# Kernel tuning notes

Measured on AMD Instinct MI355X. Metric: run time of the kernel, lower is better.

Reference implementation:

```python
import jax, jax.numpy as jnp
import numpy as np

B, T, C, H, D, W = 4, 4096, 1024, 16, 64, 128  # batch, seq, n_embd, n_head, head_dim, window
NB = T // W  # number of query blocks
EPS = 1e-6


def _rms(x, w):
    # RMSNorm over last dim
    return x * jax.lax.rsqrt(jnp.mean(x * x, axis=-1, keepdims=True) + EPS) * w


def _rope(x, pos_ids):
    # MRoPE: pos_ids [T,3]; axis_id maps each freq to one of 3 axes
    inv_freq = 1.0 / (1e6 ** (jnp.arange(0, D, 2, dtype=jnp.float32) / D))  # [D/2]
    axis_id = jnp.arange(D // 2) % 3
    positions = pos_ids[:, axis_id].astype(jnp.float32)  # [T, D/2]
    freqs = positions * inv_freq  # [T, D/2]
    emb = jnp.concatenate([freqs, freqs], axis=-1)  # [T, D]
    cos = jnp.cos(emb)[None, None]  # [1,1,T,D]
    sin = jnp.sin(emb)[None, None]
    x1, x2 = x[..., : D // 2], x[..., D // 2 :]
    rot = jnp.concatenate([-x2, x1], axis=-1)
    return x * cos + rot * sin


def setup_inputs() -> dict:
    key = jax.random.key(0)
    ks = jax.random.split(key, 3)
    x = jax.random.normal(ks[0], (B, T, C), jnp.float32)
    pos = jnp.arange(T, dtype=jnp.int32)
    pos_ids = jnp.stack([pos, pos, pos], axis=-1)  # [T,3] text positions
    w_attn = jax.random.normal(ks[1], (C, C + 2 * D), jnp.float32) * 0.02
    w_proj = jax.random.normal(ks[2], (C, C), jnp.float32) * 0.02
    q_norm_w = jnp.ones((D,), jnp.float32)
    k_norm_w = jnp.ones((D,), jnp.float32)
    return {"x": x, "pos_ids": pos_ids, "w_attn": w_attn, "w_proj": w_proj,
            "q_norm_w": q_norm_w, "k_norm_w": k_norm_w}


def reference(x, pos_ids, w_attn, w_proj, q_norm_w, k_norm_w):
    # fused qkv projection (torch Linear without bias; weight stored [in,out])
    qkv = x @ w_attn  # [B,T,C+2D]
    q = qkv[..., :C].reshape(B, T, H, D).transpose(0, 2, 1, 3)  # [B,H,T,D]
    k = qkv[..., C : C + D][:, None]  # [B,1,T,D] single KV head (MQA)
    v = qkv[..., C + D :][:, None]  # [B,1,T,D]
    q = _rope(_rms(q, q_norm_w), pos_ids)
    k = _rope(_rms(k, k_norm_w), pos_ids)
    # sliding-window attention (q >= kv and q - kv <= W), computed in blocks of W
    qb = q.reshape(B, H, NB, W, D)
    kb = k.reshape(B, NB, W, D)
    vb = v.reshape(B, NB, W, D)
    kp = jnp.concatenate([jnp.zeros_like(kb[:, :1]), kb[:, :-1]], axis=1)  # prev k block
    vp = jnp.concatenate([jnp.zeros_like(vb[:, :1]), vb[:, :-1]], axis=1)
    kv_k = jnp.concatenate([kp, kb], axis=2)  # [B,NB,2W,D]
    kv_v = jnp.concatenate([vp, vb], axis=2)
    n = jnp.arange(NB)[:, None, None]
    qr = jnp.arange(W)[None, :, None]
    kr = jnp.arange(2 * W)[None, None, :]
    q_abs = n * W + qr
    kv_abs = (n - 1) * W + kr
    mask = (q_abs >= kv_abs) & (q_abs - kv_abs <= W) & (kv_abs >= 0)  # [NB,W,2W]
    scores = jnp.einsum("bhnqd,bnkd->bhnqk", qb, kv_k) / jnp.sqrt(jnp.float32(D))
    scores = jnp.where(mask[None, None], scores, -1e30)
    attn = jax.nn.softmax(scores, axis=-1)
    y = jnp.einsum("bhnqk,bnkd->bhnqd", attn, kv_v)  # [B,H,NB,W,D]
    y = y.reshape(B, H, T, D).transpose(0, 2, 1, 3).reshape(B, T, C)
    return y @ w_proj
```

## Files before the change

### kernel.cpp

```cpp
#include <hip/hip_runtime.h>


typedef __attribute__((ext_vector_type(8))) short short8;
typedef __attribute__((ext_vector_type(4))) float f32x4;
typedef __attribute__((ext_vector_type(16))) float f32x16;
typedef __attribute__((ext_vector_type(4))) unsigned uint4v;

#define DEV static __device__ __forceinline__

DEV unsigned short f2bf(float f) {
  unsigned u = __builtin_bit_cast(unsigned, f);
  u += 0x7fffu + ((u >> 16) & 1u);
  return (unsigned short)(u >> 16);
}
DEV float bf2f(unsigned short s) {
  unsigned u = ((unsigned)s) << 16;
  return __builtin_bit_cast(float, u);
}
DEV unsigned cvtpk(float a, float b) {
  unsigned r;
  asm("v_cvt_pk_bf16_f32 %0, %1, %2" : "=v"(r) : "v"(a), "v"(b));
  return r;
}

DEV f32x4 mfma16(short8 a, short8 b, f32x4 c) {
  return __builtin_amdgcn_mfma_f32_16x16x32_bf16(a, b, c, 0, 0, 0);
}
DEV f32x16 mfma32(short8 a, short8 b, f32x16 c) {
  return __builtin_amdgcn_mfma_f32_32x32x16_bf16(a, b, c, 0, 0, 0);
}

DEV void gload16(const void* g, void* l) {
  __builtin_amdgcn_global_load_lds(
      (const __attribute__((address_space(1))) unsigned int*)(unsigned long long)g,
      (__attribute__((address_space(3))) unsigned int*)(unsigned int)(unsigned long long)l,
      16, 0, 0);
}

#define BARRIER __builtin_amdgcn_s_barrier()
#define LGKM0  asm volatile("s_waitcnt lgkmcnt(0)" ::: "memory")
#define VMCNT4 asm volatile("s_waitcnt vmcnt(4)" ::: "memory")

__global__ __launch_bounds__(256) void k_cvt(const float* __restrict__ in,
                                             short* __restrict__ out, int n4) {
  int i = blockIdx.x * 256 + threadIdx.x;
  if (i >= n4) return;
  float4 v = ((const float4*)in)[i];
  short4 o;
  o.x = (short)f2bf(v.x); o.y = (short)f2bf(v.y);
  o.z = (short)f2bf(v.z); o.w = (short)f2bf(v.w);
  ((short4*)out)[i] = o;
}

__global__ __launch_bounds__(256) void k_tcvt(const float* __restrict__ W,
                                              short* __restrict__ Wt, int K, int N) {
  __shared__ float tl[32][33];
  int tx = threadIdx.x & 31, ty = threadIdx.x >> 5;
  int k0 = blockIdx.x * 32, n0 = blockIdx.y * 32;
#pragma unroll
  for (int i = 0; i < 4; ++i)
    tl[ty + i * 8][tx] = W[(size_t)(k0 + ty + i * 8) * N + n0 + tx];
  __syncthreads();
#pragma unroll
  for (int i = 0; i < 4; ++i)
    Wt[(size_t)(n0 + ty + i * 8) * K + k0 + tx] = (short)f2bf(tl[tx][ty + i * 8]);
}

__global__ __launch_bounds__(256) void k_trig(const int* __restrict__ pos,
                                              float* __restrict__ tbl) {
  int idx = blockIdx.x * 256 + threadIdx.x;
  int t = idx >> 5, j = idx & 31;
  float invf = __expf((float)j * (-13.815510558f / 32.f));
  float p = (float)pos[t * 3 + (j % 3)];
  float s, c;
  sincosf(p * invf, &s, &c);
  ((float2*)tbl)[idx] = make_float2(c, s);
}

__global__ __launch_bounds__(512, 2) void k_gemm256(
    const short* __restrict__ A, const short* __restrict__ Bt,
    void* __restrict__ Cout, int M, int N, int K, int outBf16,
    const float* __restrict__ trig,
    const float* __restrict__ qw, const float* __restrict__ kw,
    short* __restrict__ qb2, short* __restrict__ kb2, short* __restrict__ vtg,
    int mode) {
  __shared__ short sm[65536];
  int nbn = N >> 8;
  int nwg = (M >> 8) * nbn;
  int bid = blockIdx.x;
  int swz = (bid & 7) * (nwg >> 3) + (bid >> 3);
  int bm = swz / nbn, bn = swz % nbn;
  int tid = threadIdx.x, wid = tid >> 6, lane = tid & 63;
  int wm = wid >> 2, wn = wid & 3;
  int lo = lane & 15, hi = lane >> 4;
  int NT = K >> 6;

  int r0 = tid >> 3, dc = tid & 7;
  int sc = dc ^ (r0 & 7);
  const short* aS0 = A  + (size_t)(bm * 256 + r0) * K + sc * 8;
  const short* bS0 = Bt + (size_t)(bn * 256 + r0) * K + sc * 8;
  size_t hstep = (size_t)128 * K;

  auto stage = [&](int jt, int mat, int h, int d) {
    const short* s = (mat ? bS0 : aS0) + (size_t)h * hstep + jt * 64;
    short* l = sm + d * 32768 + mat * 16384 + h * 8192;
    gload16(s,                     l + tid * 8);
    gload16(s + (size_t)64 * K,    l + 4096 + tid * 8);
  };

  int aRd[2];
#pragma unroll
  for (int kk = 0; kk < 2; ++kk)
    aRd[kk] = lo * 64 + (((kk << 2) | hi) ^ (lo & 7)) * 8;

  short8 Afr[8][2];
  short8 Bfr[2][2];
  f32x4 acc[8][4] = {};

  auto rdA = [&](int d, int m0) {
    int base = d * 32768 + wm * 8192;
#pragma unroll
    for (int m = 0; m < 4; ++m)
#pragma unroll
      for (int kk = 0; kk < 2; ++kk)
        Afr[m0 + m][kk] = *(const short8*)&sm[base + (m0 + m) * 1024 + aRd[kk]];
  };
  auto rdB = [&](int d, int n0) {
    int base = d * 32768 + 16384 + (wn >> 1) * 8192 + (wn & 1) * 4096;
#pragma unroll
    for (int nf = 0; nf < 2; ++nf)
#pragma unroll
      for (int kk = 0; kk < 2; ++kk)
        Bfr[nf][kk] = *(const short8*)&sm[base + (n0 + nf) * 1024 + aRd[kk]];
  };
  auto quad = [&](int m0, int n0) {
    __builtin_amdgcn_s_setprio(1);
#pragma unroll
    for (int m = 0; m < 4; ++m)
#pragma unroll
      for (int j = 0; j < 2; ++j)
#pragma unroll
        for (int kk = 0; kk < 2; ++kk)
          acc[m0 + m][n0 + j] = mfma16(Afr[m0 + m][kk], Bfr[j][kk], acc[m0 + m][n0 + j]);
    __builtin_amdgcn_s_setprio(0);
  };

  stage(0, 0, 0, 0); stage(0, 1, 0, 0); stage(0, 0, 1, 0); stage(0, 1, 1, 0);
  if (NT > 1) { stage(1, 0, 0, 1); stage(1, 1, 0, 1); }
  VMCNT4;
  BARRIER;

#pragma unroll 2
  for (int jt = 0; jt < NT; ++jt) {
    int d = jt & 1;
    rdA(d, 0); rdB(d, 0);
    if (jt + 1 < NT) stage(jt + 1, 0, 1, d ^ 1);
    BARRIER; LGKM0;
    quad(0, 0);
    BARRIER;
    rdA(d, 4);
    if (jt + 1 < NT) stage(jt + 1, 1, 1, d ^ 1);
    BARRIER; LGKM0;
    quad(4, 0);
    BARRIER;
    rdB(d, 2);
    if (jt + 2 < NT) stage(jt + 2, 0, 0, d);
    BARRIER; LGKM0;
    quad(0, 2);
    BARRIER;
    if (jt + 2 < NT) stage(jt + 2, 1, 0, d);
    VMCNT4;
    BARRIER;
    quad(4, 2);
    BARRIER;
  }

  if (mode == 1) {
    int tg0 = (bm * 256 + wm * 128) & 4095;
    int bb  = (bm * 256) >> 12;
    bool isQ = bn < 4, isK = (bn == 4 && wn == 0), isV = (bn == 4 && wn == 1);
    if (isQ || isK) {
      const float* nw = isQ ? qw : kw;
      float w0 = nw[lo], w1 = nw[16 + lo], w2 = nw[32 + lo], w3 = nw[48 + lo];
      short* dst = isQ ? qb2 + (size_t)((bb * 16 + bn * 4 + wn) * 4096) * 64
                       : kb2 + (size_t)(bb * 4096) * 64;
      const float2* tb = (const float2*)trig;
#pragma unroll
      for (int m = 0; m < 8; ++m)
#pragma unroll
        for (int r = 0; r < 4; ++r) {
          float x0 = acc[m][0][r], x1 = acc[m][1][r];
          float x2 = acc[m][2][r], x3 = acc[m][3][r];
          float ss = x0 * x0 + x1 * x1 + x2 * x2 + x3 * x3;
          ss += __shfl_xor(ss, 1); ss += __shfl_xor(ss, 2);
          ss += __shfl_xor(ss, 4); ss += __shfl_xor(ss, 8);
          float rn = rsqrtf(ss * 0.015625f + 1e-6f);
          x0 *= rn * w0; x1 *= rn * w1; x2 *= rn * w2; x3 *= rn * w3;
          int tp = tg0 + m * 16 + hi * 4 + r;
          float2 cs0 = tb[tp * 32 + lo];
          float2 cs1 = tb[tp * 32 + 16 + lo];
          float o0 = x0 * cs0.x - x2 * cs0.y;
          float o1 = x1 * cs1.x - x3 * cs1.y;
          float o2 = x2 * cs0.x + x0 * cs0.y;
          float o3 = x3 * cs1.x + x1 * cs1.y;
          size_t tb_ = (size_t)tp * 64;
          dst[tb_ + lo]      = (short)f2bf(o0);
          dst[tb_ + 16 + lo] = (short)f2bf(o1);
          dst[tb_ + 32 + lo] = (short)f2bf(o2);
          dst[tb_ + 48 + lo] = (short)f2bf(o3);
        }
    } else if (isV) {
#pragma unroll
      for (int m = 0; m < 8; ++m)
#pragma unroll
        for (int nf = 0; nf < 4; ++nf) {
          int dd = nf * 16 + lo;
          short4 o;
          o.x = (short)f2bf(acc[m][nf][0]);
          o.y = (short)f2bf(acc[m][nf][1]);
          o.z = (short)f2bf(acc[m][nf][2]);
          o.w = (short)f2bf(acc[m][nf][3]);
          *(short4*)&vtg[((size_t)(bb * 64 + dd)) * 4096 + tg0 + m * 16 + hi * 4] = o;
        }
    }
    return;
  }

  int row0 = bm * 256 + wm * 128 + hi * 4;
  int col0 = bn * 256 + wn * 64 + lo;
  if (outBf16) {
    short* C = (short*)Cout;
#pragma unroll
    for (int m = 0; m < 8; ++m)
#pragma unroll
      for (int nf = 0; nf < 4; ++nf)
#pragma unroll
        for (int r = 0; r < 4; ++r)
          C[(size_t)(row0 + m * 16 + r) * N + col0 + nf * 16] = (short)f2bf(acc[m][nf][r]);
  } else {
    float* C = (float*)Cout;
#pragma unroll
    for (int m = 0; m < 8; ++m)
#pragma unroll
      for (int nf = 0; nf < 4; ++nf)
#pragma unroll
        for (int r = 0; r < 4; ++r)
          C[(size_t)(row0 + m * 16 + r) * N + col0 + nf * 16] = acc[m][nf][r];
  }
}

__global__ __launch_bounds__(256, 4) void k_attn(const short* __restrict__ qb,
                                                 const short* __restrict__ kb,
                                                 const short* __restrict__ vtg,
                                                 short* __restrict__ y) {
  __shared__ __align__(16) char smem[33792];
  short* ks  = (short*)smem;
  short* vts = (short*)(smem + 16384);
  int bid = blockIdx.x;
  int swz = (bid & 7) * 256 + (bid >> 3);
  int h = swz & 15, n = (swz >> 4) & 31, b = swz >> 9;
  int tid = threadIdx.x, wid = tid >> 6, lane = tid & 63;
  int lo = lane & 31, hi = lane >> 5;

  const short* qrow = qb + (size_t)((b * 16 + h) * 4096 + n * 128 + wid * 32 + lo) * 64;
  short8 aq[4];
#pragma unroll
  for (int s = 0; s < 4; ++s) aq[s] = *(const short8*)(qrow + s * 16 + hi * 8);

  f32x16 O0 = {}, O1 = {};
  float mrun = -1e30f, lrun = 0.f;
  int qr = wid * 32 + lo;
  const float SC = 0.125f * 1.4426950408889634f;

  for (int hf = (n == 0) ? 1 : 0; hf < 2; ++hf) {
    int tg = (n - 1 + hf) * 128;
#pragma unroll
    for (int p = 0; p < 4; ++p) {
      int idx = p * 256 + tid;
      int r = idx >> 3, dc = idx & 7;
      gload16(kb + (size_t)(b * 4096 + tg + r) * 64 + ((dc ^ (r & 7)) << 3),
              ks + idx * 8);
    }
#pragma unroll
    for (int p = 0; p < 4; ++p) {
      int idx = p * 256 + tid;
      int dd = idx >> 4, s = idx & 15;
      gload16(vtg + (size_t)(b * 64 + dd) * 4096 + tg + ((s ^ (dd & 7)) << 3),
              vts + idx * 8);
    }
    __syncthreads();

#pragma unroll
    for (int mt = 0; mt < 4; ++mt) {
      f32x16 S = {};
      int r = mt * 32 + lo;
#pragma unroll
      for (int kst = 0; kst < 4; ++kst) {
        short8 kf = *(const short8*)&ks[r * 64 + ((((kst << 1) | hi) ^ (r & 7)) << 3)];
        S = mfma32(kf, aq[kst], S);
      }
#pragma unroll
      for (int rr = 0; rr < 16; ++rr) {
        int kg = hf * 128 + mt * 32 + (rr & 3) + ((rr >> 2) << 3) + (hi << 2);
        S[rr] = (kg >= qr && kg <= qr + 128) ? S[rr] * SC : -30000.f;
      }
      float pmax = S[0];
#pragma unroll
      for (int rr = 1; rr < 16; ++rr) pmax = fmaxf(pmax, S[rr]);
      pmax = fmaxf(pmax, __shfl_xor(pmax, 32));
      if (!__all(pmax - mrun <= 8.f)) {
        float mn = fmaxf(mrun, pmax);
        float al = exp2f(mrun - mn);
        lrun *= al; mrun = mn;
#pragma unroll
        for (int rr = 0; rr < 16; ++rr) { O0[rr] *= al; O1[rr] *= al; }
      }
      float ls = 0.f;
#pragma unroll
      for (int rr = 0; rr < 16; ++rr) { S[rr] = exp2f(S[rr] - mrun); ls += S[rr]; }
      ls += __shfl_xor(ls, 32);
      lrun += ls;
#pragma unroll
      for (int h2 = 0; h2 < 2; ++h2) {
        int b0 = h2 * 8;
        unsigned pk0 = cvtpk(S[b0 + 0], S[b0 + 1]);
        unsigned pk1 = cvtpk(S[b0 + 2], S[b0 + 3]);
        unsigned pk2 = cvtpk(S[b0 + 4], S[b0 + 5]);
        unsigned pk3 = cvtpk(S[b0 + 6], S[b0 + 7]);
        asm("v_permlane32_swap_b32 %0, %1" : "+v"(pk0), "+v"(pk2));
        asm("v_permlane32_swap_b32 %0, %1" : "+v"(pk1), "+v"(pk3));
        uint4v uw; uw.x = pk0; uw.y = pk1; uw.z = pk2; uw.w = pk3;
        short8 pb = __builtin_bit_cast(short8, uw);
        int kc = mt * 4 + h2 * 2 + hi;
        short8 vb0 = *(const short8*)&vts[lo * 128 + ((kc ^ (lo & 7)) << 3)];
        short8 vb1 = *(const short8*)&vts[(32 + lo) * 128 + ((kc ^ (lo & 7)) << 3)];
        O0 = mfma32(vb0, pb, O0);
        O1 = mfma32(vb1, pb, O1);
      }
    }
    __syncthreads();
  }

  float inv = 1.f / lrun;
  float* ot = (float*)smem + wid * 2112;
#pragma unroll
  for (int r = 0; r < 16; ++r) {
    int d0 = (r & 3) + ((r >> 2) << 3) + (hi << 2);
    ot[d0 * 33 + lo]        = O0[r] * inv;
    ot[(d0 + 32) * 33 + lo] = O1[r] * inv;
  }
  __syncthreads();
  int tok = lane >> 3, dc = lane & 7;
#pragma unroll
  for (int g = 0; g < 4; ++g) {
    int q = g * 8 + tok;
    short8 o8;
#pragma unroll
    for (int jj = 0; jj < 8; ++jj)
      o8[jj] = (short)f2bf(ot[(dc * 8 + jj) * 33 + q]);
    *(short8*)&y[(size_t)(b * 4096 + n * 128 + wid * 32 + q) * 1024 + h * 64 + dc * 8] = o8;
  }
}

extern "C" void kernel_launch(void* const* d_in, const int* in_sizes, int n_in,
                              void* d_out, int out_size, void* d_ws, size_t ws_size,
                              hipStream_t stream) {
  const float* x      = (const float*)d_in[0];
  const int*   pos    = (const int*)d_in[1];
  const float* w_attn = (const float*)d_in[2];
  const float* w_proj = (const float*)d_in[3];
  const float* qw     = (const float*)d_in[4];
  const float* kw     = (const float*)d_in[5];

  char* ws = (char*)d_ws;
  short* xb   = (short*)ws;
  short* wabt = (short*)(ws + 33554432);
  short* wpbt = (short*)(ws + 36175872);
  short* qb2  = (short*)(ws + 38273024);
  short* kb2  = (short*)(ws + 71827456);
  short* vtg  = (short*)(ws + 73924608);
  float* trig = (float*)(ws + 76021760);
  short* ybuf = xb;

  hipLaunchKernelGGL(k_cvt, dim3(16384), dim3(256), 0, stream, x, xb, 4194304);
  hipLaunchKernelGGL(k_tcvt, dim3(32, 36), dim3(256), 0, stream, w_attn, wabt, 1024, 1152);
  hipLaunchKernelGGL(k_tcvt, dim3(32, 32), dim3(256), 0, stream, w_proj, wpbt, 1024, 1024);
  hipLaunchKernelGGL(k_trig, dim3(512), dim3(256), 0, stream, pos, trig);
  hipLaunchKernelGGL(k_gemm256, dim3(320), dim3(512), 0, stream, xb, wabt,
                     (void*)nullptr, 16384, 1280, 1024, 1,
                     trig, qw, kw, qb2, kb2, vtg, 1);
  hipLaunchKernelGGL(k_attn, dim3(2048), dim3(256), 0, stream, qb2, kb2, vtg, ybuf);
  hipLaunchKernelGGL(k_gemm256, dim3(256), dim3(512), 0, stream, ybuf, wpbt, d_out,
                     16384, 1024, 1024, 0,
                     (const float*)nullptr, (const float*)nullptr,
                     (const float*)nullptr,
                     (short*)nullptr, (short*)nullptr, (short*)nullptr, 0);
}
```

Measured before the change: 175.5 us.

## Split K/V projection into a dedicated small GEMM to drop padded columns

The fused QKV GEMM previously ran with N padded to 1280, wasting a 256-wide column tile of which only 128 columns (K and V) were needed. Q is now computed by the large GEMM with N=1024, and a new smaller 128x128-tile kernel computes K/V with RMSNorm, RoPE and the V transpose in its epilogue. This removes wasted MFMA work but adds an extra, unpipelined kernel launch serialized before the main GEMM. The workspace offsets are tightened to match the actual weight size.

```diff
diff --git a/kernel.cpp b/kernel.cpp
--- a/kernel.cpp
+++ b/kernel.cpp
@@ -77,13 +77,93 @@
   ((float2*)tbl)[idx] = make_float2(c, s);
 }
 
+__global__ __launch_bounds__(256) void k_gemmkv(const short* __restrict__ A,
+                                                const short* __restrict__ Bt,
+                                                const float* __restrict__ trig,
+                                                const float* __restrict__ kw,
+                                                short* __restrict__ kb2,
+                                                short* __restrict__ vtg) {
+  __shared__ short As[128 * 32];
+  __shared__ short Bs[128 * 32];
+  const int K = 1024;
+  int bid = blockIdx.x;
+  int bm = (bid & 7) * 16 + (bid >> 3);
+  int tid = threadIdx.x, lane = tid & 63, wid = tid >> 6;
+  int wr = wid >> 1, wc = wid & 1;
+  int lo = lane & 15, hi = lane >> 4;
+  const short* Ab = A + (size_t)(bm * 128 + (tid >> 2)) * K + (tid & 3) * 8;
+  const short* Bb = Bt + (size_t)(tid >> 2) * K + (tid & 3) * 8;
+  f32x4 acc[4][4] = {};
+  for (int kt = 0; kt < K; kt += 32) {
+    gload16(Ab + kt,            As + tid * 8);
+    gload16(Ab + kt + 64 * K,   As + 2048 + tid * 8);
+    gload16(Bb + kt,            Bs + tid * 8);
+    gload16(Bb + kt + 64 * K,   Bs + 2048 + tid * 8);
+    __syncthreads();
+    short8 a[4], b[4];
+#pragma unroll
+    for (int m = 0; m < 4; ++m)
+      a[m] = *(const short8*)&As[(wr * 64 + m * 16 + lo) * 32 + hi * 8];
+#pragma unroll
+    for (int n = 0; n < 4; ++n)
+      b[n] = *(const short8*)&Bs[(wc * 64 + n * 16 + lo) * 32 + hi * 8];
+#pragma unroll
+    for (int m = 0; m < 4; ++m)
+#pragma unroll
+      for (int n = 0; n < 4; ++n)
+        acc[m][n] = mfma16(a[m], b[n], acc[m][n]);
+    __syncthreads();
+  }
+  int tg0 = (bm * 128 + wr * 64) & 4095;
+  int bb  = (bm * 128) >> 12;
+  if (wc == 0) {
+    float w0 = kw[lo], w1 = kw[16 + lo], w2 = kw[32 + lo], w3 = kw[48 + lo];
+    const float2* tb = (const float2*)trig;
+#pragma unroll
+    for (int m = 0; m < 4; ++m)
+#pragma unroll
+      for (int r = 0; r < 4; ++r) {
+        float x0 = acc[m][0][r], x1 = acc[m][1][r];
+        float x2 = acc[m][2][r], x3 = acc[m][3][r];
+        float ss = x0 * x0 + x1 * x1 + x2 * x2 + x3 * x3;
+        ss += __shfl_xor(ss, 1); ss += __shfl_xor(ss, 2);
+        ss += __shfl_xor(ss, 4); ss += __shfl_xor(ss, 8);
+        float rn = rsqrtf(ss * 0.015625f + 1e-6f);
+        x0 *= rn * w0; x1 *= rn * w1; x2 *= rn * w2; x3 *= rn * w3;
+        int tp = tg0 + m * 16 + hi * 4 + r;
+        float2 cs0 = tb[tp * 32 + lo];
+        float2 cs1 = tb[tp * 32 + 16 + lo];
+        float o0 = x0 * cs0.x - x2 * cs0.y;
+        float o1 = x1 * cs1.x - x3 * cs1.y;
+        float o2 = x2 * cs0.x + x0 * cs0.y;
+        float o3 = x3 * cs1.x + x1 * cs1.y;
+        size_t tb_ = ((size_t)bb * 4096 + tp) * 64;
+        kb2[tb_ + lo]      = (short)f2bf(o0);
+        kb2[tb_ + 16 + lo] = (short)f2bf(o1);
+        kb2[tb_ + 32 + lo] = (short)f2bf(o2);
+        kb2[tb_ + 48 + lo] = (short)f2bf(o3);
+      }
+  } else {
+#pragma unroll
+    for (int m = 0; m < 4; ++m)
+#pragma unroll
+      for (int nf = 0; nf < 4; ++nf) {
+        int dd = nf * 16 + lo;
+        short4 o;
+        o.x = (short)f2bf(acc[m][nf][0]);
+        o.y = (short)f2bf(acc[m][nf][1]);
+        o.z = (short)f2bf(acc[m][nf][2]);
+        o.w = (short)f2bf(acc[m][nf][3]);
+        *(short4*)&vtg[((size_t)(bb * 64 + dd)) * 4096 + tg0 + m * 16 + hi * 4] = o;
+      }
+  }
+}
+
 __global__ __launch_bounds__(512, 2) void k_gemm256(
     const short* __restrict__ A, const short* __restrict__ Bt,
     void* __restrict__ Cout, int M, int N, int K, int outBf16,
-    const float* __restrict__ trig,
-    const float* __restrict__ qw, const float* __restrict__ kw,
-    short* __restrict__ qb2, short* __restrict__ kb2, short* __restrict__ vtg,
-    int mode) {
+    const float* __restrict__ trig, const float* __restrict__ qw,
+    short* __restrict__ qb2, int mode) {
   __shared__ short sm[65536];
   int nbn = N >> 8;
   int nwg = (M >> 8) * nbn;
@@ -178,51 +258,34 @@
   if (mode == 1) {
     int tg0 = (bm * 256 + wm * 128) & 4095;
     int bb  = (bm * 256) >> 12;
-    bool isQ = bn < 4, isK = (bn == 4 && wn == 0), isV = (bn == 4 && wn == 1);
-    if (isQ || isK) {
-      const float* nw = isQ ? qw : kw;
-      float w0 = nw[lo], w1 = nw[16 + lo], w2 = nw[32 + lo], w3 = nw[48 + lo];
-      short* dst = isQ ? qb2 + (size_t)((bb * 16 + bn * 4 + wn) * 4096) * 64
-                       : kb2 + (size_t)(bb * 4096) * 64;
-      const float2* tb = (const float2*)trig;
-#pragma unroll
-      for (int m = 0; m < 8; ++m)
-#pragma unroll
-        for (int r = 0; r < 4; ++r) {
-          float x0 = acc[m][0][r], x1 = acc[m][1][r];
-          float x2 = acc[m][2][r], x3 = acc[m][3][r];
-          float ss = x0 * x0 + x1 * x1 + x2 * x2 + x3 * x3;
-          ss += __shfl_xor(ss, 1); ss += __shfl_xor(ss, 2);
-          ss += __shfl_xor(ss, 4); ss += __shfl_xor(ss, 8);
-          float rn = rsqrtf(ss * 0.015625f + 1e-6f);
-          x0 *= rn * w0; x1 *= rn * w1; x2 *= rn * w2; x3 *= rn * w3;
-          int tp = tg0 + m * 16 + hi * 4 + r;
-          float2 cs0 = tb[tp * 32 + lo];
-          float2 cs1 = tb[tp * 32 + 16 + lo];
-          float o0 = x0 * cs0.x - x2 * cs0.y;
-          float o1 = x1 * cs1.x - x3 * cs1.y;
-          float o2 = x2 * cs0.x + x0 * cs0.y;
-          float o3 = x3 * cs1.x + x1 * cs1.y;
-          size_t tb_ = (size_t)tp * 64;
-          dst[tb_ + lo]      = (short)f2bf(o0);
-          dst[tb_ + 16 + lo] = (short)f2bf(o1);
-          dst[tb_ + 32 + lo] = (short)f2bf(o2);
-          dst[tb_ + 48 + lo] = (short)f2bf(o3);
-        }
-    } else if (isV) {
-#pragma unroll
-      for (int m = 0; m < 8; ++m)
-#pragma unroll
-        for (int nf = 0; nf < 4; ++nf) {
-          int dd = nf * 16 + lo;
-          short4 o;
-          o.x = (short)f2bf(acc[m][nf][0]);
-          o.y = (short)f2bf(acc[m][nf][1]);
-          o.z = (short)f2bf(acc[m][nf][2]);
-          o.w = (short)f2bf(acc[m][nf][3]);
-          *(short4*)&vtg[((size_t)(bb * 64 + dd)) * 4096 + tg0 + m * 16 + hi * 4] = o;
-        }
-    }
+    int hh  = bn * 4 + wn;
+    float w0 = qw[lo], w1 = qw[16 + lo], w2 = qw[32 + lo], w3 = qw[48 + lo];
+    short* dst = qb2 + (size_t)((bb * 16 + hh) * 4096) * 64;
+    const float2* tb = (const float2*)trig;
+#pragma unroll
+    for (int m = 0; m < 8; ++m)
+#pragma unroll
+      for (int r = 0; r < 4; ++r) {
+        float x0 = acc[m][0][r], x1 = acc[m][1][r];
+        float x2 = acc[m][2][r], x3 = acc[m][3][r];
+        float ss = x0 * x0 + x1 * x1 + x2 * x2 + x3 * x3;
+        ss += __shfl_xor(ss, 1); ss += __shfl_xor(ss, 2);
+        ss += __shfl_xor(ss, 4); ss += __shfl_xor(ss, 8);
+        float rn = rsqrtf(ss * 0.015625f + 1e-6f);
+        x0 *= rn * w0; x1 *= rn * w1; x2 *= rn * w2; x3 *= rn * w3;
+        int tp = tg0 + m * 16 + hi * 4 + r;
+        float2 cs0 = tb[tp * 32 + lo];
+        float2 cs1 = tb[tp * 32 + 16 + lo];
+        float o0 = x0 * cs0.x - x2 * cs0.y;
+        float o1 = x1 * cs1.x - x3 * cs1.y;
+        float o2 = x2 * cs0.x + x0 * cs0.y;
+        float o3 = x3 * cs1.x + x1 * cs1.y;
+        size_t tb_ = (size_t)tp * 64;
+        dst[tb_ + lo]      = (short)f2bf(o0);
+        dst[tb_ + 16 + lo] = (short)f2bf(o1);
+        dst[tb_ + 32 + lo] = (short)f2bf(o2);
+        dst[tb_ + 48 + lo] = (short)f2bf(o3);
+      }
     return;
   }
 
@@ -375,24 +438,24 @@
   char* ws = (char*)d_ws;
   short* xb   = (short*)ws;
   short* wabt = (short*)(ws + 33554432);
-  short* wpbt = (short*)(ws + 36175872);
-  short* qb2  = (short*)(ws + 38273024);
-  short* kb2  = (short*)(ws + 71827456);
-  short* vtg  = (short*)(ws + 73924608);
-  float* trig = (float*)(ws + 76021760);
+  short* wpbt = (short*)(ws + 35913728);
+  short* qb2  = (short*)(ws + 38010880);
+  short* kb2  = (short*)(ws + 71565312);
+  short* vtg  = (short*)(ws + 73662464);
+  float* trig = (float*)(ws + 75759616);
   short* ybuf = xb;
 
   hipLaunchKernelGGL(k_cvt, dim3(16384), dim3(256), 0, stream, x, xb, 4194304);
   hipLaunchKernelGGL(k_tcvt, dim3(32, 36), dim3(256), 0, stream, w_attn, wabt, 1024, 1152);
   hipLaunchKernelGGL(k_tcvt, dim3(32, 32), dim3(256), 0, stream, w_proj, wpbt, 1024, 1024);
   hipLaunchKernelGGL(k_trig, dim3(512), dim3(256), 0, stream, pos, trig);
-  hipLaunchKernelGGL(k_gemm256, dim3(320), dim3(512), 0, stream, xb, wabt,
-                     (void*)nullptr, 16384, 1280, 1024, 1,
-                     trig, qw, kw, qb2, kb2, vtg, 1);
+  hipLaunchKernelGGL(k_gemmkv, dim3(128), dim3(256), 0, stream, xb,
+                     wabt + (size_t)1024 * 1024, trig, kw, kb2, vtg);
+  hipLaunchKernelGGL(k_gemm256, dim3(256), dim3(512), 0, stream, xb, wabt,
+                     (void*)nullptr, 16384, 1024, 1024, 1, trig, qw, qb2, 1);
   hipLaunchKernelGGL(k_attn, dim3(2048), dim3(256), 0, stream, qb2, kb2, vtg, ybuf);
   hipLaunchKernelGGL(k_gemm256, dim3(256), dim3(512), 0, stream, ybuf, wpbt, d_out,
                      16384, 1024, 1024, 0,
                      (const float*)nullptr, (const float*)nullptr,
-                     (const float*)nullptr,
-                     (short*)nullptr, (short*)nullptr, (short*)nullptr, 0);
-}
+                     (short*)nullptr, 0);
+}
```

After: 167.7 us. 4.5% less time.
